# Optimization experiments

Measured on AMD Instinct MI355X. Metric: run time of the kernel, lower is better.

Reference implementation:

```python
import jax, jax.numpy as jnp
import numpy as np

B, V, C, H, W, D = 1, 3, 32, 320, 320, 32


def setup_inputs() -> dict:
    key = jax.random.key(0)
    ks = jax.random.split(key, 14)
    feats = jax.random.normal(ks[0], (B, V, C, H, W), jnp.float32)
    # Valid pinhole projections: P = [[K @ [R|t]], [0,0,0,1]], identity rotation,
    # horizontal baselines sized so the warp stays mostly in-image over the depth range.
    K = np.array([[400.0, 0.0, W / 2.0], [0.0, 400.0, H / 2.0], [0.0, 0.0, 1.0]])
    mats = []
    for tx in (0.0, 100.0, -100.0):
        Rt = np.eye(4)
        Rt[0, 3] = tx
        P = np.eye(4)
        P[:3, :4] = K @ Rt[:3, :4]
        mats.append(P)
    proj = jnp.asarray(np.broadcast_to(np.stack(mats)[None], (B, V, 4, 4)).copy(), jnp.float32)
    planes = jnp.linspace(425.0, 935.0, D, dtype=jnp.float32)
    depth_values = jnp.broadcast_to(planes[None, :, None, None], (B, D, H, W)).astype(jnp.float32)
    s = 0.05  # small init so exp(reg_cost) stays well-scaled
    W0 = s * jax.random.normal(ks[1], (8, C, 3, 3), jnp.float32)
    Ws1 = s * jax.random.normal(ks[2], (8, 8, 3, 3), jnp.float32)
    W1 = s * jax.random.normal(ks[3], (16, 8, 3, 3), jnp.float32)
    Ws2 = s * jax.random.normal(ks[4], (16, 16, 3, 3), jnp.float32)
    W2 = s * jax.random.normal(ks[5], (32, 16, 3, 3), jnp.float32)
    Ws3 = s * jax.random.normal(ks[6], (32, 32, 3, 3), jnp.float32)
    W3 = s * jax.random.normal(ks[7], (64, 32, 3, 3), jnp.float32)
    Ws4 = s * jax.random.normal(ks[8], (64, 64, 3, 3), jnp.float32)
    U4 = s * jax.random.normal(ks[9], (32, 64, 1, 1), jnp.float32)
    U3 = s * jax.random.normal(ks[10], (16, 32, 1, 1), jnp.float32)
    U2 = s * jax.random.normal(ks[11], (8, 16, 1, 1), jnp.float32)
    Wout = s * jax.random.normal(ks[12], (1, 8, 3, 3), jnp.float32)
    return dict(feats=feats, proj=proj, depth_values=depth_values, W0=W0, Ws1=Ws1,
                W1=W1, Ws2=Ws2, W2=W2, Ws3=Ws3, W3=W3, Ws4=Ws4, U4=U4, U3=U3, U2=U2, Wout=Wout)


def _conv(x, w, stride=1):
    return jax.lax.conv_general_dilated(x, w, (stride, stride), 'SAME',
                                        dimension_numbers=('NCHW', 'OIHW', 'NCHW'))


def _up2(x):
    return jnp.repeat(jnp.repeat(x, 2, axis=2), 2, axis=3)


def _bilinear(img, x, y):
    # img [C,H,W]; x,y [N] pixel coords; zero padding, align_corners semantics
    Cc, Hh, Ww = img.shape
    x0 = jnp.floor(x)
    y0 = jnp.floor(y)
    wx = x - x0
    wy = y - y0

    def tap(xi, yi):
        valid = ((xi >= 0) & (xi <= Ww - 1) & (yi >= 0) & (yi <= Hh - 1)).astype(img.dtype)
        xc = jnp.clip(xi, 0, Ww - 1).astype(jnp.int32)
        yc = jnp.clip(yi, 0, Hh - 1).astype(jnp.int32)
        return img[:, yc, xc] * valid  # [C,N]

    return (tap(x0, y0) * (1 - wx) * (1 - wy) + tap(x0 + 1, y0) * wx * (1 - wy)
            + tap(x0, y0 + 1) * (1 - wx) * wy + tap(x0 + 1, y0 + 1) * wx * wy)


def _forward(feats, proj, depth_values, W0, Ws1, W1, Ws2, W2, Ws3, W3, Ws4, U4, U3, U2, Wout):
    Bn, Vn, Cn, Hn, Wn = feats.shape
    Dn = depth_values.shape[1]
    N = Hn * Wn
    relu = jax.nn.relu
    ref = feats[:, 0]
    ref_sq = ref * ref
    # Precompute per-src-view rotated pixel rays and translations.
    inv_ref = jnp.linalg.inv(proj[:, 0])                       # [B,4,4]
    rel = jnp.einsum('bvij,bjk->bvik', proj[:, 1:], inv_ref)   # [B,V-1,4,4]
    rot, trans = rel[:, :, :3, :3], rel[:, :, :3, 3]
    ys, xs = jnp.meshgrid(jnp.arange(Hn), jnp.arange(Wn), indexing='ij')
    pix = jnp.stack([xs.ravel(), ys.ravel(), jnp.ones(N)], 0).astype(feats.dtype)  # [3,N]
    rot_pix = jnp.einsum('bvij,jn->bvin', rot, pix)            # [B,V-1,3,N]

    def regularize(x, s1, s2, s3, s4):
        c1 = relu(_conv(x, W0) + _conv(s1, Ws1))
        c2 = relu(_conv(c1, W1, 2) + _conv(s2, Ws2))
        c3 = relu(_conv(c2, W2, 2) + _conv(s3, Ws3))
        c4 = relu(_conv(c3, W3, 2) + _conv(s4, Ws4))
        u3 = c3 + _up2(_conv(c4, U4))
        u2 = c2 + _up2(_conv(u3, U3))
        u1 = c1 + _up2(_conv(u2, U2))
        return _conv(u1, Wout), c1, c2, c3, c4

    def step(carry, depth_slice):  # depth_slice [B,H,W]
        s1, s2, s3, s4, exp_sum, depth_img, max_prob = carry
        vol_sum, vol_sq = ref, ref_sq
        dflat = depth_slice.reshape(Bn, 1, N)
        for v in range(Vn - 1):
            xyz = rot_pix[:, v] * dflat + trans[:, v, :, None]   # [B,3,N]
            px = xyz[:, 0] / xyz[:, 2]
            py = xyz[:, 1] / xyz[:, 2]
            warped = jax.vmap(_bilinear)(feats[:, v + 1], px, py).reshape(Bn, Cn, Hn, Wn)
            vol_sum = vol_sum + warped
            vol_sq = vol_sq + warped * warped
        variance = vol_sq / Vn - (vol_sum / Vn) ** 2
        cost, s1, s2, s3, s4 = regularize(variance, s1, s2, s3, s4)
        prob = jnp.exp(cost)                                     # [B,1,H,W]
        max_prob = jnp.maximum(max_prob, prob)                   # == flag*prob + (1-flag)*max
        depth_img = depth_img + depth_slice[:, None] * prob
        exp_sum = exp_sum + prob
        return (s1, s2, s3, s4, exp_sum, depth_img, max_prob), None

    z = lambda c, h, w: jnp.zeros((Bn, c, h, w), feats.dtype)
    init = (z(8, Hn, Wn), z(16, Hn // 2, Wn // 2), z(32, Hn // 4, Wn // 4), z(64, Hn // 8, Wn // 8),
            z(1, Hn, Wn), z(1, Hn, Wn), z(1, Hn, Wn))
    carry, _ = jax.lax.scan(step, init, jnp.moveaxis(depth_values, 1, 0))
    _, _, _, _, exp_sum, depth_img, max_prob = carry
    es = exp_sum + 1e-10
    depth_map = (depth_img / es)[:, 0]
    prob_map = (max_prob / es)[:, 0]
    return jnp.stack([depth_map, prob_map], axis=1)  # [B,2,H,W]


def reference(feats, proj, depth_values, W0, Ws1, W1, Ws2, W2, Ws3, W3, Ws4, U4, U3, U2, Wout):
    return _forward(feats, proj, depth_values, W0, Ws1, W1, Ws2, W2, Ws3, W3, Ws4, U4, U3, U2, Wout)
```

## Files before the change

kernel.cpp:

```cpp
#include <hip/hip_runtime.h>
#include <hip/hip_bf16.h>
#include <math.h>

#define HH 320
#define WW 320
#define NP (HH*WW)
#define CC 32
#define DD 32

#define H2 160
#define W2 160
#define N2 (H2*W2)
#define H4 80
#define W4 80
#define N4 (H4*W4)
#define H8 40
#define W8 40
#define N8 (H8*W8)

#define HALO 18
#define NHALO (HALO*HALO)

#define C1SZ (8*NP)
#define C2SZ (16*N2)
#define C3SZ (32*N4)
#define C4SZ (64*N8)

#define OFF_REL   0
#define OFF_C1R   64
#define OFF_C2R   (OFF_C1R + 5*C1SZ)
#define OFF_C3R   (OFF_C2R + 4*C2SZ)
#define OFF_C4R   (OFF_C3R + 3*C3SZ)
#define OFF_ESUM  (OFF_C4R + 2*C4SZ)
#define OFF_DIMG  (OFF_ESUM + NP)
#define OFF_MAXP  (OFF_DIMG + NP)
#define OFF_END   (OFF_MAXP + NP)

__global__ void k_prep(const float* __restrict__ proj, float* __restrict__ rel) {
    if (threadIdx.x != 0 || blockIdx.x != 0) return;
    double a[4][8];
    for (int i = 0; i < 4; i++)
        for (int j = 0; j < 4; j++) {
            a[i][j] = (double)proj[i*4 + j];
            a[i][j+4] = (i == j) ? 1.0 : 0.0;
        }
    for (int c = 0; c < 4; c++) {
        int pv = c; double best = fabs(a[c][c]);
        for (int r = c+1; r < 4; r++) {
            double v = fabs(a[r][c]);
            if (v > best) { best = v; pv = r; }
        }
        if (pv != c)
            for (int j = 0; j < 8; j++) { double t = a[c][j]; a[c][j] = a[pv][j]; a[pv][j] = t; }
        double inv = 1.0 / a[c][c];
        for (int j = 0; j < 8; j++) a[c][j] *= inv;
        for (int r = 0; r < 4; r++) if (r != c) {
            double f = a[r][c];
            for (int j = 0; j < 8; j++) a[r][j] -= f * a[c][j];
        }
    }
    for (int v = 1; v < 3; v++) {
        const float* P = proj + v*16;
        double rm[4][4];
        for (int i = 0; i < 4; i++)
            for (int j = 0; j < 4; j++) {
                double s = 0.0;
                for (int k = 0; k < 4; k++) s += (double)P[i*4 + k] * a[k][j+4];
                rm[i][j] = s;
            }
        float* o = rel + (v-1)*12;
        o[0]=(float)rm[0][0]; o[1]=(float)rm[0][1]; o[2]=(float)rm[0][2];
        o[3]=(float)rm[1][0]; o[4]=(float)rm[1][1]; o[5]=(float)rm[1][2];
        o[6]=(float)rm[2][0]; o[7]=(float)rm[2][1]; o[8]=(float)rm[2][2];
        o[9]=(float)rm[0][3]; o[10]=(float)rm[1][3]; o[11]=(float)rm[2][3];
    }
}


__device__ void stageA(int blk, int d,
        const float* __restrict__ feats, const float* __restrict__ rel,
        const float* __restrict__ depthv, const float* __restrict__ c1r,
        const float* __restrict__ W0, const float* __restrict__ Ws1,
        float* smem) {
    float* vs = smem;
    float* ss = smem + 32*NHALO;
    const float* dslice = depthv + (size_t)d * NP;
    const float* s1 = c1r + (size_t)((d+4)%5) * C1SZ;
    float* c1out = (float*)c1r + (size_t)(d%5) * C1SZ;

    int bx = blk % 20, by = blk / 20;
    int ox0 = bx*16, oy0 = by*16;

    const float* f0 = feats;
    const float* f1 = feats + CC*NP;
    const float* f2 = feats + 2*CC*NP;
    const float inv3 = 1.0f / 3.0f;

    for (int hp = threadIdx.x; hp < NHALO; hp += 256) {
        int hy = hp / HALO, hx = hp - hy*HALO;
        int gy = oy0 + hy - 1, gx = ox0 + hx - 1;
        if (gy < 0 || gy >= HH || gx < 0 || gx >= WW) {
#pragma unroll
            for (int c = 0; c < 32; c++) vs[c*NHALO + hp] = 0.0f;
#pragma unroll
            for (int c = 0; c < 8; c++) ss[c*NHALO + hp] = 0.0f;
        } else {
            int p = gy*WW + gx;
            float depth = dslice[p];
            float fx = (float)gx, fy = (float)gy;
            int offs[8]; float wts[8];
#pragma unroll
            for (int v = 0; v < 2; v++) {
                const float* r = rel + v*12;
                float X = (r[0]*fx + r[1]*fy + r[2]) * depth + r[9];
                float Y = (r[3]*fx + r[4]*fy + r[5]) * depth + r[10];
                float Z = (r[6]*fx + r[7]*fy + r[8]) * depth + r[11];
                float iz = 1.0f / Z;
                float px = X * iz, py = Y * iz;
                float x0f = floorf(px), y0f = floorf(py);
                float wx = px - x0f, wy = py - y0f;
                int x0 = (int)x0f, y0 = (int)y0f;
#pragma unroll
                for (int t = 0; t < 4; t++) {
                    int xi = x0 + (t & 1), yi = y0 + (t >> 1);
                    float wgt = ((t & 1) ? wx : 1.0f - wx) * ((t >> 1) ? wy : 1.0f - wy);
                    bool valid = (xi >= 0) && (xi <= WW-1) && (yi >= 0) && (yi <= HH-1);
                    int xc = min(max(xi, 0), WW-1);
                    int yc = min(max(yi, 0), HH-1);
                    offs[v*4 + t] = yc*WW + xc;
                    wts[v*4 + t] = valid ? wgt : 0.0f;
                }
            }
#pragma unroll 4
            for (int c = 0; c < 32; c++) {
                float rv = f0[c*NP + p];
                float sum = rv, sq = rv * rv;
                const float* b1 = f1 + c*NP;
                float t1 = b1[offs[0]]*wts[0] + b1[offs[1]]*wts[1] + b1[offs[2]]*wts[2] + b1[offs[3]]*wts[3];
                const float* b2 = f2 + c*NP;
                float t2 = b2[offs[4]]*wts[4] + b2[offs[5]]*wts[5] + b2[offs[6]]*wts[6] + b2[offs[7]]*wts[7];
                sum += t1 + t2;
                sq  += t1*t1 + t2*t2;
                float m = sum * inv3;
                vs[c*NHALO + hp] = sq * inv3 - m*m;
            }
#pragma unroll
            for (int c = 0; c < 8; c++) ss[c*NHALO + hp] = s1[c*NP + p];
        }
    }
    __syncthreads();

    int px = threadIdx.x & 15, py = threadIdx.x >> 4;
    int base = py*HALO + px;
    float acc[8];
#pragma unroll
    for (int o = 0; o < 8; o++) acc[o] = 0.0f;
    for (int ci = 0; ci < 32; ci++) {
        float t[9];
#pragma unroll
        for (int ky = 0; ky < 3; ky++)
#pragma unroll
            for (int kx = 0; kx < 3; kx++) t[ky*3+kx] = vs[ci*NHALO + base + ky*HALO + kx];
#pragma unroll
        for (int o = 0; o < 8; o++) {
            const float* w = W0 + (o*32 + ci)*9;
            float a = acc[o];
#pragma unroll
            for (int k = 0; k < 9; k++) a += t[k] * w[k];
            acc[o] = a;
        }
    }
    for (int ci = 0; ci < 8; ci++) {
        float t[9];
#pragma unroll
        for (int ky = 0; ky < 3; ky++)
#pragma unroll
            for (int kx = 0; kx < 3; kx++) t[ky*3+kx] = ss[ci*NHALO + base + ky*HALO + kx];
#pragma unroll
        for (int o = 0; o < 8; o++) {
            const float* w = Ws1 + (o*8 + ci)*9;
            float a = acc[o];
#pragma unroll
            for (int k = 0; k < 9; k++) a += t[k] * w[k];
            acc[o] = a;
        }
    }
    int p = (oy0 + py)*WW + ox0 + px;
#pragma unroll
    for (int o = 0; o < 8; o++) c1out[o*NP + p] = fmaxf(acc[o], 0.0f);
}

__device__ void stageB(int blk, int d,
        const float* __restrict__ c1r, const float* __restrict__ c2r_,
        const float* __restrict__ W1, const float* __restrict__ Ws2) {
    const float* c1 = c1r + (size_t)(d%5) * C1SZ;
    const float* s2 = c2r_ + (size_t)((d+3)%4) * C2SZ;
    float* c2 = (float*)c2r_ + (size_t)(d%4) * C2SZ;
    int p = (blk % 100)*256 + threadIdx.x;
    if (p >= N2) return;
    int og = blk / 100;
    int y = p / W2, x = p - y*W2;
    int offsA[9]; float mskA[9];
#pragma unroll
    for (int k = 0; k < 9; k++) {
        int yy = 2*y + k/3, xx = 2*x + k%3;
        bool v = (yy < HH) && (xx < WW);
        offsA[k] = v ? yy*WW + xx : 0;
        mskA[k] = v ? 1.0f : 0.0f;
    }
    int offsB[9]; float mskB[9];
#pragma unroll
    for (int k = 0; k < 9; k++) {
        int yy = y + k/3 - 1, xx = x + k%3 - 1;
        bool v = (yy >= 0) && (yy < H2) && (xx >= 0) && (xx < W2);
        offsB[k] = v ? yy*W2 + xx : 0;
        mskB[k] = v ? 1.0f : 0.0f;
    }
    float acc[4];
#pragma unroll
    for (int o = 0; o < 4; o++) acc[o] = 0.0f;
    for (int ci = 0; ci < 8; ci++) {
        const float* b = c1 + ci*NP;
        float t[9];
#pragma unroll
        for (int k = 0; k < 9; k++) t[k] = b[offsA[k]] * mskA[k];
#pragma unroll
        for (int o = 0; o < 4; o++) {
            const float* w = W1 + ((og*4 + o)*8 + ci)*9;
            float a = acc[o];
#pragma unroll
            for (int k = 0; k < 9; k++) a += t[k] * w[k];
            acc[o] = a;
        }
    }
    for (int ci = 0; ci < 16; ci++) {
        const float* b = s2 + ci*N2;
        float t[9];
#pragma unroll
        for (int k = 0; k < 9; k++) t[k] = b[offsB[k]] * mskB[k];
#pragma unroll
        for (int o = 0; o < 4; o++) {
            const float* w = Ws2 + ((og*4 + o)*16 + ci)*9;
            float a = acc[o];
#pragma unroll
            for (int k = 0; k < 9; k++) a += t[k] * w[k];
            acc[o] = a;
        }
    }
#pragma unroll
    for (int o = 0; o < 4; o++) c2[(og*4 + o)*N2 + p] = fmaxf(acc[o], 0.0f);
}

__device__ void stageC(int blk, int d,
        const float* __restrict__ c2r_, const float* __restrict__ c3r_,
        const float* __restrict__ W2w, const float* __restrict__ Ws3) {
    const float* c2 = c2r_ + (size_t)(d%4) * C2SZ;
    const float* s3 = c3r_ + (size_t)((d+2)%3) * C3SZ;
    float* c3 = (float*)c3r_ + (size_t)(d%3) * C3SZ;
    int p = (blk % 25)*256 + threadIdx.x;
    if (p >= N4) return;
    int og = blk / 25;
    int y = p / W4, x = p - y*W4;
    int offsA[9]; float mskA[9];
#pragma unroll
    for (int k = 0; k < 9; k++) {
        int yy = 2*y + k/3, xx = 2*x + k%3;
        bool v = (yy < H2) && (xx < W2);
        offsA[k] = v ? yy*W2 + xx : 0;
        mskA[k] = v ? 1.0f : 0.0f;
    }
    int offsB[9]; float mskB[9];
#pragma unroll
    for (int k = 0; k < 9; k++) {
        int yy = y + k/3 - 1, xx = x + k%3 - 1;
        bool v = (yy >= 0) && (yy < H4) && (xx >= 0) && (xx < W4);
        offsB[k] = v ? yy*W4 + xx : 0;
        mskB[k] = v ? 1.0f : 0.0f;
    }
    float acc[4];
#pragma unroll
    for (int o = 0; o < 4; o++) acc[o] = 0.0f;
    for (int ci = 0; ci < 16; ci++) {
        const float* b = c2 + ci*N2;
        float t[9];
#pragma unroll
        for (int k = 0; k < 9; k++) t[k] = b[offsA[k]] * mskA[k];
#pragma unroll
        for (int o = 0; o < 4; o++) {
            const float* w = W2w + ((og*4 + o)*16 + ci)*9;
            float a = acc[o];
#pragma unroll
            for (int k = 0; k < 9; k++) a += t[k] * w[k];
            acc[o] = a;
        }
    }
    for (int ci = 0; ci < 32; ci++) {
        const float* b = s3 + ci*N4;
        float t[9];
#pragma unroll
        for (int k = 0; k < 9; k++) t[k] = b[offsB[k]] * mskB[k];
#pragma unroll
        for (int o = 0; o < 4; o++) {
            const float* w = Ws3 + ((og*4 + o)*32 + ci)*9;
            float a = acc[o];
#pragma unroll
            for (int k = 0; k < 9; k++) a += t[k] * w[k];
            acc[o] = a;
        }
    }
#pragma unroll
    for (int o = 0; o < 4; o++) c3[(og*4 + o)*N4 + p] = fmaxf(acc[o], 0.0f);
}

__device__ void stageD(int blk, int d,
        const float* __restrict__ c3r_, const float* __restrict__ c4r_,
        const float* __restrict__ W3w, const float* __restrict__ Ws4) {
    const float* c3 = c3r_ + (size_t)(d%3) * C3SZ;
    const float* s4 = c4r_ + (size_t)((d+1)%2) * C4SZ;
    float* c4 = (float*)c4r_ + (size_t)(d%2) * C4SZ;
    int p = (blk % 7)*256 + threadIdx.x;
    if (p >= N8) return;
    int og = blk / 7;
    int y = p / W8, x = p - y*W8;
    int offsA[9]; float mskA[9];
#pragma unroll
    for (int k = 0; k < 9; k++) {
        int yy = 2*y + k/3, xx = 2*x + k%3;
        bool v = (yy < H4) && (xx < W4);
        offsA[k] = v ? yy*W4 + xx : 0;
        mskA[k] = v ? 1.0f : 0.0f;
    }
    int offsB[9]; float mskB[9];
#pragma unroll
    for (int k = 0; k < 9; k++) {
        int yy = y + k/3 - 1, xx = x + k%3 - 1;
        bool v = (yy >= 0) && (yy < H8) && (xx >= 0) && (xx < W8);
        offsB[k] = v ? yy*W8 + xx : 0;
        mskB[k] = v ? 1.0f : 0.0f;
    }
    float acc[4];
#pragma unroll
    for (int o = 0; o < 4; o++) acc[o] = 0.0f;
    for (int ci = 0; ci < 32; ci++) {
        const float* b = c3 + ci*N4;
        float t[9];
#pragma unroll
        for (int k = 0; k < 9; k++) t[k] = b[offsA[k]] * mskA[k];
#pragma unroll
        for (int o = 0; o < 4; o++) {
            const float* w = W3w + ((og*4 + o)*32 + ci)*9;
            float a = acc[o];
#pragma unroll
            for (int k = 0; k < 9; k++) a += t[k] * w[k];
            acc[o] = a;
        }
    }
    for (int ci = 0; ci < 64; ci++) {
        const float* b = s4 + ci*N8;
        float t[9];
#pragma unroll
        for (int k = 0; k < 9; k++) t[k] = b[offsB[k]] * mskB[k];
#pragma unroll
        for (int o = 0; o < 4; o++) {
            const float* w = Ws4 + ((og*4 + o)*64 + ci)*9;
            float a = acc[o];
#pragma unroll
            for (int k = 0; k < 9; k++) a += t[k] * w[k];
            acc[o] = a;
        }
    }
#pragma unroll
    for (int o = 0; o < 4; o++) c4[(og*4 + o)*N8 + p] = fmaxf(acc[o], 0.0f);
}

__device__ void stageU(int blk, int d,
        const float* __restrict__ c1r, const float* __restrict__ c2r_,
        const float* __restrict__ c3r_, const float* __restrict__ c4r_,
        const float* __restrict__ U4, const float* __restrict__ U3,
        const float* __restrict__ U2, const float* __restrict__ Wout,
        const float* __restrict__ depthv,
        float* __restrict__ exp_sum, float* __restrict__ depth_img,
        float* __restrict__ max_prob, float* smem) {
    const float* c1 = c1r + (size_t)(d%5) * C1SZ;
    const float* c2 = c2r_ + (size_t)(d%4) * C2SZ;
    const float* c3 = c3r_ + (size_t)(d%3) * C3SZ;
    const float* c4 = c4r_ + (size_t)(d%2) * C4SZ;
    const float* dslice = depthv + (size_t)d * NP;
    float* u3s = smem;
    float* u2s = smem + 32*36;
    float* u1s = smem + 32*36 + 16*100;

    int bx = blk % 20, by = blk / 20;
    int ox0 = bx*16, oy0 = by*16;
    int qy0 = (oy0 >> 2) - 1, qx0 = (ox0 >> 2) - 1;
    int hy0 = (oy0 >> 1) - 1, hx0 = (ox0 >> 1) - 1;

    for (int i = threadIdx.x; i < 32*36; i += 256) {
        int ch = i / 36, pp = i - ch*36;
        int y4 = qy0 + pp/6, x4 = qx0 + pp%6;
        int y4c = min(max(y4, 0), H4-1), x4c = min(max(x4, 0), W4-1);
        int pl = (y4c >> 1)*W8 + (x4c >> 1);
        const float* w = U4 + ch*64;
        float s = c3[ch*N4 + y4c*W4 + x4c];
#pragma unroll 8
        for (int ci = 0; ci < 64; ci++) s += c4[ci*N8 + pl] * w[ci];
        u3s[ch*36 + pp] = s;
    }
    __syncthreads();
    for (int i = threadIdx.x; i < 16*100; i += 256) {
        int ch = i / 100, pp = i - ch*100;
        int y2 = hy0 + pp/10, x2 = hx0 + pp%10;
        int y2c = min(max(y2, 0), H2-1), x2c = min(max(x2, 0), W2-1);
        int ly = (y2c >> 1) - qy0, lx = (x2c >> 1) - qx0;
        const float* w = U3 + ch*32;
        float s = c2[ch*N2 + y2c*W2 + x2c];
#pragma unroll 8
        for (int ci = 0; ci < 32; ci++) s += u3s[ci*36 + ly*6 + lx] * w[ci];
        u2s[ch*100 + pp] = s;
    }
    __syncthreads();
    for (int i = threadIdx.x; i < 8*NHALO; i += 256) {
        int ch = i / NHALO, pp = i - ch*NHALO;
        int gy = oy0 + pp/HALO - 1, gx = ox0 + pp%HALO - 1;
        float s = 0.0f;
        if (gy >= 0 && gy < HH && gx >= 0 && gx < WW) {
            int ly = (gy >> 1) - hy0, lx = (gx >> 1) - hx0;
            const float* w = U2 + ch*16;
            s = c1[ch*NP + gy*WW + gx];
#pragma unroll
            for (int ci = 0; ci < 16; ci++) s += u2s[ci*100 + ly*10 + lx] * w[ci];
        }
        u1s[ch*NHALO + pp] = s;
    }
    __syncthreads();
    int px = threadIdx.x & 15, py = threadIdx.x >> 4;
    int base = py*HALO + px;
    float cost = 0.0f;
#pragma unroll
    for (int ci = 0; ci < 8; ci++) {
        const float* w = Wout + ci*9;
#pragma unroll
        for (int ky = 0; ky < 3; ky++)
#pragma unroll
            for (int kx = 0; kx < 3; kx++)
                cost += u1s[ci*NHALO + base + ky*HALO + kx] * w[ky*3 + kx];
    }
    int p = (oy0 + py)*WW + ox0 + px;
    float prob = expf(cost);
    exp_sum[p] += prob;
    depth_img[p] += dslice[p] * prob;
    max_prob[p] = fmaxf(max_prob[p], prob);
}

__global__ __launch_bounds__(256) void k_uber(
        int t,
        const float* __restrict__ feats, const float* __restrict__ rel,
        const float* __restrict__ depthv,
        const float* __restrict__ W0, const float* __restrict__ Ws1,
        const float* __restrict__ W1, const float* __restrict__ Ws2,
        const float* __restrict__ W2w, const float* __restrict__ Ws3,
        const float* __restrict__ W3w, const float* __restrict__ Ws4,
        const float* __restrict__ U4, const float* __restrict__ U3,
        const float* __restrict__ U2, const float* __restrict__ Wout,
        float* __restrict__ c1r, float* __restrict__ c2r,
        float* __restrict__ c3r, float* __restrict__ c4r,
        float* __restrict__ esum, float* __restrict__ dimg,
        float* __restrict__ maxp) {
    __shared__ float smem[32*NHALO + 8*NHALO];
    int b = blockIdx.x;
    if (b < 400) {
        int d = t;
        if (d < DD) stageA(b, d, feats, rel, depthv, c1r, W0, Ws1, smem);
    } else if (b < 800) {
        int d = t - 1;
        if (d >= 0 && d < DD) stageB(b - 400, d, c1r, c2r, W1, Ws2);
    } else if (b < 1000) {
        int d = t - 2;
        if (d >= 0 && d < DD) stageC(b - 800, d, c2r, c3r, W2w, Ws3);
    } else if (b < 1112) {
        int d = t - 3;
        if (d >= 0 && d < DD) stageD(b - 1000, d, c3r, c4r, W3w, Ws4);
    } else {
        int d = t - 4;
        if (d >= 0 && d < DD)
            stageU(b - 1112, d, c1r, c2r, c3r, c4r, U4, U3, U2, Wout, depthv,
                   esum, dimg, maxp, smem);
    }
}

__global__ __launch_bounds__(256) void k_final(
        const float* __restrict__ exp_sum, const float* __restrict__ depth_img,
        const float* __restrict__ max_prob, float* __restrict__ out) {
    int p = blockIdx.x*256 + threadIdx.x;
    if (p >= NP) return;
    float es = exp_sum[p] + 1e-10f;
    out[p] = depth_img[p] / es;
    out[NP + p] = max_prob[p] / es;
}

extern "C" void kernel_launch(void* const* d_in, const int* in_sizes, int n_in,
                              void* d_out, int out_size, void* d_ws, size_t ws_size,
                              hipStream_t stream) {
    const float* feats = (const float*)d_in[0];
    const float* proj  = (const float*)d_in[1];
    const float* depthv= (const float*)d_in[2];
    const float* W0  = (const float*)d_in[3];
    const float* Ws1 = (const float*)d_in[4];
    const float* W1  = (const float*)d_in[5];
    const float* Ws2 = (const float*)d_in[6];
    const float* W2w = (const float*)d_in[7];
    const float* Ws3 = (const float*)d_in[8];
    const float* W3w = (const float*)d_in[9];
    const float* Ws4 = (const float*)d_in[10];
    const float* U4  = (const float*)d_in[11];
    const float* U3  = (const float*)d_in[12];
    const float* U2  = (const float*)d_in[13];
    const float* Wout= (const float*)d_in[14];

    float* ws = (float*)d_ws;
    float* rel  = ws + OFF_REL;
    float* c1r  = ws + OFF_C1R;
    float* c2r  = ws + OFF_C2R;
    float* c3r  = ws + OFF_C3R;
    float* c4r  = ws + OFF_C4R;
    float* esum = ws + OFF_ESUM;
    float* dimg = ws + OFF_DIMG;
    float* maxp = ws + OFF_MAXP;

    hipMemsetAsync(c1r, 0, (size_t)(OFF_END - OFF_C1R) * sizeof(float), stream);
    k_prep<<<1, 1, 0, stream>>>(proj, rel);

    for (int t = 0; t < DD + 4; t++) {
        k_uber<<<dim3(1512), 256, 0, stream>>>(t, feats, rel, depthv,
            W0, Ws1, W1, Ws2, W2w, Ws3, W3w, Ws4, U4, U3, U2, Wout,
            c1r, c2r, c3r, c4r, esum, dimg, maxp);
    }
    k_final<<<dim3(400), 256, 0, stream>>>(esum, dimg, maxp, (float*)d_out);
}
```

Baseline: 3.173 ms.

## Chunk stage-A variance channels to shrink shared memory footprint

Stage A now builds the variance halo tile in four chunks of 8 channels, running the 3x3 conv on each chunk before loading the next, then reuses the same buffer for the skip input. This cuts the uber kernel's shared memory from 40 channel-halo planes to roughly 11 planes' worth, so more blocks can be resident per CU. The cost is that the projection and bilinear-offset math is recomputed for every chunk, and there are extra barriers.

```diff
diff --git a/kernel.cpp b/kernel.cpp
--- a/kernel.cpp
+++ b/kernel.cpp
@@ -25,6 +25,8 @@
 #define C2SZ (16*N2)
 #define C3SZ (32*N4)
 #define C4SZ (64*N8)
+
+#define SMEM_FLOATS (32*36 + 16*100 + 8*NHALO)
 
 #define OFF_REL   0
 #define OFF_C1R   64
@@ -81,9 +83,7 @@
         const float* __restrict__ feats, const float* __restrict__ rel,
         const float* __restrict__ depthv, const float* __restrict__ c1r,
         const float* __restrict__ W0, const float* __restrict__ Ws1,
-        float* smem) {
-    float* vs = smem;
-    float* ss = smem + 32*NHALO;
+        float* buf) {
     const float* dslice = depthv + (size_t)d * NP;
     const float* s1 = c1r + (size_t)((d+4)%5) * C1SZ;
     float* c1out = (float*)c1r + (size_t)(d%5) * C1SZ;
@@ -91,91 +91,103 @@
     int bx = blk % 20, by = blk / 20;
     int ox0 = bx*16, oy0 = by*16;
 
-    const float* f0 = feats;
     const float* f1 = feats + CC*NP;
     const float* f2 = feats + 2*CC*NP;
     const float inv3 = 1.0f / 3.0f;
 
+    int opx = threadIdx.x & 15, opy = threadIdx.x >> 4;
+    int obase = opy*HALO + opx;
+    int outp = (oy0 + opy)*WW + ox0 + opx;
+
+    float acc[8];
+#pragma unroll
+    for (int o = 0; o < 8; o++) acc[o] = 0.0f;
+
+    for (int chunk = 0; chunk < 4; chunk++) {
+        int cbase = chunk*8;
+        for (int hp = threadIdx.x; hp < NHALO; hp += 256) {
+            int hy = hp / HALO, hx = hp - hy*HALO;
+            int gy = oy0 + hy - 1, gx = ox0 + hx - 1;
+            if (gy < 0 || gy >= HH || gx < 0 || gx >= WW) {
+#pragma unroll
+                for (int c = 0; c < 8; c++) buf[c*NHALO + hp] = 0.0f;
+            } else {
+                int p = gy*WW + gx;
+                float depth = dslice[p];
+                float fx = (float)gx, fy = (float)gy;
+                int offs[8]; float wts[8];
+#pragma unroll
+                for (int v = 0; v < 2; v++) {
+                    const float* r = rel + v*12;
+                    float X = (r[0]*fx + r[1]*fy + r[2]) * depth + r[9];
+                    float Y = (r[3]*fx + r[4]*fy + r[5]) * depth + r[10];
+                    float Z = (r[6]*fx + r[7]*fy + r[8]) * depth + r[11];
+                    float iz = 1.0f / Z;
+                    float px = X * iz, py = Y * iz;
+                    float x0f = floorf(px), y0f = floorf(py);
+                    float wx = px - x0f, wy = py - y0f;
+                    int x0 = (int)x0f, y0 = (int)y0f;
+#pragma unroll
+                    for (int t = 0; t < 4; t++) {
+                        int xi = x0 + (t & 1), yi = y0 + (t >> 1);
+                        float wgt = ((t & 1) ? wx : 1.0f - wx) * ((t >> 1) ? wy : 1.0f - wy);
+                        bool valid = (xi >= 0) && (xi <= WW-1) && (yi >= 0) && (yi <= HH-1);
+                        int xc = min(max(xi, 0), WW-1);
+                        int yc = min(max(yi, 0), HH-1);
+                        offs[v*4 + t] = yc*WW + xc;
+                        wts[v*4 + t] = valid ? wgt : 0.0f;
+                    }
+                }
+#pragma unroll
+                for (int c = 0; c < 8; c++) {
+                    int cg = cbase + c;
+                    float rv = feats[cg*NP + p];
+                    float sum = rv, sq = rv * rv;
+                    const float* b1 = f1 + cg*NP;
+                    float t1 = b1[offs[0]]*wts[0] + b1[offs[1]]*wts[1] + b1[offs[2]]*wts[2] + b1[offs[3]]*wts[3];
+                    const float* b2 = f2 + cg*NP;
+                    float t2 = b2[offs[4]]*wts[4] + b2[offs[5]]*wts[5] + b2[offs[6]]*wts[6] + b2[offs[7]]*wts[7];
+                    sum += t1 + t2;
+                    sq  += t1*t1 + t2*t2;
+                    float m = sum * inv3;
+                    buf[c*NHALO + hp] = sq * inv3 - m*m;
+                }
+            }
+        }
+        __syncthreads();
+        for (int ci = 0; ci < 8; ci++) {
+            float t[9];
+#pragma unroll
+            for (int ky = 0; ky < 3; ky++)
+#pragma unroll
+                for (int kx = 0; kx < 3; kx++) t[ky*3+kx] = buf[ci*NHALO + obase + ky*HALO + kx];
+#pragma unroll
+            for (int o = 0; o < 8; o++) {
+                const float* w = W0 + (o*32 + cbase + ci)*9;
+                float a = acc[o];
+#pragma unroll
+                for (int k = 0; k < 9; k++) a += t[k] * w[k];
+                acc[o] = a;
+            }
+        }
+        __syncthreads();
+    }
+
     for (int hp = threadIdx.x; hp < NHALO; hp += 256) {
         int hy = hp / HALO, hx = hp - hy*HALO;
         int gy = oy0 + hy - 1, gx = ox0 + hx - 1;
-        if (gy < 0 || gy >= HH || gx < 0 || gx >= WW) {
-#pragma unroll
-            for (int c = 0; c < 32; c++) vs[c*NHALO + hp] = 0.0f;
-#pragma unroll
-            for (int c = 0; c < 8; c++) ss[c*NHALO + hp] = 0.0f;
-        } else {
-            int p = gy*WW + gx;
-            float depth = dslice[p];
-            float fx = (float)gx, fy = (float)gy;
-            int offs[8]; float wts[8];
-#pragma unroll
-            for (int v = 0; v < 2; v++) {
-                const float* r = rel + v*12;
-                float X = (r[0]*fx + r[1]*fy + r[2]) * depth + r[9];
-                float Y = (r[3]*fx + r[4]*fy + r[5]) * depth + r[10];
-                float Z = (r[6]*fx + r[7]*fy + r[8]) * depth + r[11];
-                float iz = 1.0f / Z;
-                float px = X * iz, py = Y * iz;
-                float x0f = floorf(px), y0f = floorf(py);
-                float wx = px - x0f, wy = py - y0f;
-                int x0 = (int)x0f, y0 = (int)y0f;
-#pragma unroll
-                for (int t = 0; t < 4; t++) {
-                    int xi = x0 + (t & 1), yi = y0 + (t >> 1);
-                    float wgt = ((t & 1) ? wx : 1.0f - wx) * ((t >> 1) ? wy : 1.0f - wy);
-                    bool valid = (xi >= 0) && (xi <= WW-1) && (yi >= 0) && (yi <= HH-1);
-                    int xc = min(max(xi, 0), WW-1);
-                    int yc = min(max(yi, 0), HH-1);
-                    offs[v*4 + t] = yc*WW + xc;
-                    wts[v*4 + t] = valid ? wgt : 0.0f;
-                }
-            }
-#pragma unroll 4
-            for (int c = 0; c < 32; c++) {
-                float rv = f0[c*NP + p];
-                float sum = rv, sq = rv * rv;
-                const float* b1 = f1 + c*NP;
-                float t1 = b1[offs[0]]*wts[0] + b1[offs[1]]*wts[1] + b1[offs[2]]*wts[2] + b1[offs[3]]*wts[3];
-                const float* b2 = f2 + c*NP;
-                float t2 = b2[offs[4]]*wts[4] + b2[offs[5]]*wts[5] + b2[offs[6]]*wts[6] + b2[offs[7]]*wts[7];
-                sum += t1 + t2;
-                sq  += t1*t1 + t2*t2;
-                float m = sum * inv3;
-                vs[c*NHALO + hp] = sq * inv3 - m*m;
-            }
-#pragma unroll
-            for (int c = 0; c < 8; c++) ss[c*NHALO + hp] = s1[c*NP + p];
-        }
+        bool v = (gy >= 0) && (gy < HH) && (gx >= 0) && (gx < WW);
+        int p = v ? gy*WW + gx : 0;
+#pragma unroll
+        for (int c = 0; c < 8; c++) buf[c*NHALO + hp] = v ? s1[c*NP + p] : 0.0f;
     }
     __syncthreads();
-
-    int px = threadIdx.x & 15, py = threadIdx.x >> 4;
-    int base = py*HALO + px;
-    float acc[8];
-#pragma unroll
-    for (int o = 0; o < 8; o++) acc[o] = 0.0f;
-    for (int ci = 0; ci < 32; ci++) {
+    for (int ci = 0; ci < 8; ci++) {
         float t[9];
 #pragma unroll
         for (int ky = 0; ky < 3; ky++)
 #pragma unroll
-            for (int kx = 0; kx < 3; kx++) t[ky*3+kx] = vs[ci*NHALO + base + ky*HALO + kx];
-#pragma unroll
-        for (int o = 0; o < 8; o++) {
-            const float* w = W0 + (o*32 + ci)*9;
-            float a = acc[o];
-#pragma unroll
-            for (int k = 0; k < 9; k++) a += t[k] * w[k];
-            acc[o] = a;
-        }
-    }
-    for (int ci = 0; ci < 8; ci++) {
-        float t[9];
-#pragma unroll
-        for (int ky = 0; ky < 3; ky++)
-#pragma unroll
-            for (int kx = 0; kx < 3; kx++) t[ky*3+kx] = ss[ci*NHALO + base + ky*HALO + kx];
+            for (int kx = 0; kx < 3; kx++) t[ky*3+kx] = buf[ci*NHALO + obase + ky*HALO + kx];
 #pragma unroll
         for (int o = 0; o < 8; o++) {
             const float* w = Ws1 + (o*8 + ci)*9;
@@ -185,9 +197,8 @@
             acc[o] = a;
         }
     }
-    int p = (oy0 + py)*WW + ox0 + px;
-#pragma unroll
-    for (int o = 0; o < 8; o++) c1out[o*NP + p] = fmaxf(acc[o], 0.0f);
+#pragma unroll
+    for (int o = 0; o < 8; o++) c1out[o*NP + outp] = fmaxf(acc[o], 0.0f);
 }
 
 __device__ void stageB(int blk, int d,
@@ -466,7 +477,7 @@
         float* __restrict__ c3r, float* __restrict__ c4r,
         float* __restrict__ esum, float* __restrict__ dimg,
         float* __restrict__ maxp) {
-    __shared__ float smem[32*NHALO + 8*NHALO];
+    __shared__ float smem[SMEM_FLOATS];
     int b = blockIdx.x;
     if (b < 400) {
         int d = t;
```

New measurement: 2.994 ms. 1.06x faster.
